# Kernel tuning notes

Hardware: AMD Instinct MI355X
Metric: run time of the kernel (lower is better)

## Reference

```python
import jax, jax.numpy as jnp
import numpy as np

B, G, S, NNZ = 64, 20000, 200000, 2000000

def setup_inputs() -> dict:
    key = jax.random.key(0)
    k1, k2, k3, k4, k5 = jax.random.split(key, 5)
    x = jax.random.normal(k1, (B, G), dtype=jnp.float32)
    # COO connectivity: row = SNP index (output), col = gene index (input)
    row = jax.random.randint(k2, (NNZ,), 0, S, dtype=jnp.int64)
    col = jax.random.randint(k3, (NNZ,), 0, G, dtype=jnp.int64)
    index = jnp.stack([row, col])  # [2, NNZ]
    W_sparse = jax.random.normal(k4, (NNZ,), dtype=jnp.float32) * 0.02
    b = jax.random.normal(k5, (S, 1), dtype=jnp.float32) * 0.02
    return {"x": x, "W_sparse": W_sparse, "b": b, "index": index, "n_SNPs": S}

def reference(x, W_sparse, b, index, n_SNPs):
    # spmm: sparse [n_SNPs, n_genes] @ x.T [n_genes, B] -> [n_SNPs, B]
    row, col = index[0], index[1]
    gathered = x.T[col] * W_sparse[:, None]            # [NNZ, B] edge contributions
    dot_prod = jax.ops.segment_sum(gathered, row, num_segments=n_SNPs)  # [S, B]
    output = dot_prod + b                              # bias broadcast over batch
    return output.T                                    # [B, n_SNPs]
```

## Files before the change

### kernel.cpp

```cpp
#include <hip/hip_runtime.h>
#include <hip/hip_bf16.h>


#define WAVE 64
#define BIN_EDGES 8192
#define CO_BITS 10
#define CO_ROWS 1024
#define NCO_MAX 256
#define CAP 11264

#define RL(v, i)  __builtin_amdgcn_readlane((int)(v), (i))
#define RLF(v, i) __int_as_float(__builtin_amdgcn_readlane(__float_as_int(v), (i)))

__device__ __forceinline__ int swz(int r, int b) {
    return (r << 6) + (b ^ (r & 63));
}

__device__ __forceinline__ unsigned short f2bf(float f) {
    unsigned u = __float_as_uint(f);
    unsigned r = (u + 0x7fffu + ((u >> 16) & 1u)) >> 16;
    return (unsigned short)r;
}

__global__ void initcur_kernel(int* __restrict__ bincur, int nc) {
    const int t = blockIdx.x * 256 + threadIdx.x;
    if (t < nc) bincur[t] = t * CAP;
}

__global__ void transpose64_kernel(const float* __restrict__ x,
                                   unsigned short* __restrict__ xTh, int G) {
    __shared__ float tile[64][65];
    const int t  = threadIdx.x;
    const int g0 = blockIdx.x * 64;
    {
        const int j  = t & 63;
        const int b0 = t >> 6;
        if (g0 + j < G) {
            #pragma unroll
            for (int it = 0; it < 16; ++it) {
                const int b = b0 + it * 4;
                tile[j][b] = x[(size_t)b * G + g0 + j];
            }
        }
    }
    __syncthreads();
    {
        const int b  = t & 63;
        const int j0 = t >> 6;
        #pragma unroll
        for (int it = 0; it < 16; ++it) {
            const int j = j0 + it * 4;
            if (g0 + j < G) xTh[(size_t)(g0 + j) * WAVE + b] = f2bf(tile[j][b]);
        }
    }
}

__global__ __launch_bounds__(256) void pass1_kernel(
        const int* __restrict__ row, const int* __restrict__ col,
        const float* __restrict__ w, int* __restrict__ bincur,
        uint2* __restrict__ sedge1, int nnz, int ncoarse) {
    __shared__ int hist[4][NCO_MAX];
    __shared__ int cb[NCO_MAX];
    __shared__ int cur[NCO_MAX];
    const int t  = threadIdx.x;
    const int wv = t >> 6;
    const int e0 = blockIdx.x * BIN_EDGES;
    const bool full = (e0 + BIN_EDGES <= nnz);
    for (int j = t; j < 4 * NCO_MAX; j += 256) ((int*)hist)[j] = 0;
    __syncthreads();
    if (full) {
        const int4* rv = (const int4*)(row + e0);
        #pragma unroll 2
        for (int k = 0; k < BIN_EDGES / 1024; ++k) {
            const int4 r4 = rv[k * 256 + t];
            atomicAdd(&hist[wv][r4.x >> CO_BITS], 1);
            atomicAdd(&hist[wv][r4.y >> CO_BITS], 1);
            atomicAdd(&hist[wv][r4.z >> CO_BITS], 1);
            atomicAdd(&hist[wv][r4.w >> CO_BITS], 1);
        }
    } else {
        for (int k = 0; k < BIN_EDGES / 256; ++k) {
            const int i = e0 + k * 256 + t;
            if (i < nnz) atomicAdd(&hist[wv][row[i] >> CO_BITS], 1);
        }
    }
    __syncthreads();
    for (int j = t; j < ncoarse; j += 256) {
        const int h = hist[0][j] + hist[1][j] + hist[2][j] + hist[3][j];
        cb[j]  = h ? atomicAdd(&bincur[j], h) : 0;
        cur[j] = 0;
    }
    __syncthreads();
    if (full) {
        const int4*   rv = (const int4*)(row + e0);
        const int4*   cv = (const int4*)(col + e0);
        const float4* wf = (const float4*)(w + e0);
        for (int k = 0; k < BIN_EDGES / 1024; ++k) {
            const int4   r4 = rv[k * 256 + t];
            const int4   c4 = cv[k * 256 + t];
            const float4 w4 = wf[k * 256 + t];
            {
                const int c = r4.x >> CO_BITS;
                const int pos = cb[c] + atomicAdd(&cur[c], 1);
                sedge1[pos] = make_uint2(((unsigned)(r4.x & (CO_ROWS - 1)) << 15) |
                                         (unsigned)c4.x, __float_as_uint(w4.x));
            }
            {
                const int c = r4.y >> CO_BITS;
                const int pos = cb[c] + atomicAdd(&cur[c], 1);
                sedge1[pos] = make_uint2(((unsigned)(r4.y & (CO_ROWS - 1)) << 15) |
                                         (unsigned)c4.y, __float_as_uint(w4.y));
            }
            {
                const int c = r4.z >> CO_BITS;
                const int pos = cb[c] + atomicAdd(&cur[c], 1);
                sedge1[pos] = make_uint2(((unsigned)(r4.z & (CO_ROWS - 1)) << 15) |
                                         (unsigned)c4.z, __float_as_uint(w4.z));
            }
            {
                const int c = r4.w >> CO_BITS;
                const int pos = cb[c] + atomicAdd(&cur[c], 1);
                sedge1[pos] = make_uint2(((unsigned)(r4.w & (CO_ROWS - 1)) << 15) |
                                         (unsigned)c4.w, __float_as_uint(w4.w));
            }
        }
    } else {
        for (int k = 0; k < BIN_EDGES / 256; ++k) {
            const int i = e0 + k * 256 + t;
            if (i < nnz) {
                const int r = row[i];
                const int c = r >> CO_BITS;
                const int pos = cb[c] + atomicAdd(&cur[c], 1);
                sedge1[pos] = make_uint2(((unsigned)(r & (CO_ROWS - 1)) << 15) |
                                         (unsigned)col[i], __float_as_uint(w[i]));
            }
        }
    }
}

__global__ __launch_bounds__(512) void pass2_kernel(
        const uint2* __restrict__ sedge1, const int* __restrict__ bincur,
        uint2* __restrict__ sedge2, int* __restrict__ rowse, int S) {
    __shared__ int rhist[CO_ROWS];
    __shared__ int sd[512];
    const int t  = threadIdx.x;
    const int c  = blockIdx.x;
    const int cs = c * CAP;
    const int M  = bincur[c] - cs;
    const int r0 = c << CO_BITS;
    const int nrows = min(CO_ROWS, S - r0);

    rhist[t] = 0;
    rhist[t + 512] = 0;
    __syncthreads();
    for (int i = t; i < M; i += 512)
        atomicAdd(&rhist[sedge1[cs + i].x >> 15], 1);
    __syncthreads();

    const int b2 = t * 2;
    const int u0 = rhist[b2], u1 = rhist[b2 + 1];
    const int s1 = u0, s2 = u0 + u1;
    sd[t] = s2;
    __syncthreads();
    for (int o = 1; o < 512; o <<= 1) {
        const int a = (t >= o) ? sd[t - o] : 0;
        __syncthreads();
        sd[t] += a;
        __syncthreads();
    }
    const int tex = sd[t] - s2;
    rhist[b2] = tex;
    rhist[b2 + 1] = tex + s1;
    if (b2 < nrows) {
        rowse[2 * (r0 + b2)]     = cs + tex;
        rowse[2 * (r0 + b2) + 1] = cs + tex + u0;
    }
    if (b2 + 1 < nrows) {
        rowse[2 * (r0 + b2 + 1)]     = cs + tex + u0;
        rowse[2 * (r0 + b2 + 1) + 1] = cs + tex + s2;
    }
    __syncthreads();

    for (int i = t; i < M; i += 512) {
        const uint2 e = sedge1[cs + i];
        const int r = (int)(e.x >> 15);
        const int pos = cs + atomicAdd(&rhist[r], 1);
        sedge2[pos] = make_uint2((e.x & 0x7fffu) << 7, e.y);
    }
}

#define PROC(Er, ar, ii)                                                      \
    {                                                                         \
        const int   k_ = RL((Er).x, (ii));                                    \
        const float w_ = __int_as_float(RL((Er).y, (ii)));                    \
        const float v_ = __uint_as_float(                                     \
            (unsigned)*(const unsigned short*)(xb + k_ + lane2) << 16);       \
        (ar) += v_ * w_;                                                      \
    }

__global__ __launch_bounds__(256) void compute_kernel(
        const unsigned short* __restrict__ xTh,
        const uint2* __restrict__ sedge,
        const int* __restrict__ rowse,
        const float* __restrict__ bias,
        float* __restrict__ out, int S) {
    __shared__ float tile[64 * 64];
    const int lane = threadIdx.x & 63;
    const int wv   = threadIdx.x >> 6;
    const int r0   = blockIdx.x * 64;
    const int rw   = r0 + wv * 16;
    const char* xb = (const char*)xTh;
    const int lane2 = lane * 2;

    int se = 0;
    if (lane < 32) se = rowse[2 * rw + lane];
    float bv = 0.f;
    if (lane < 16) bv = bias[rw + lane];

    #pragma unroll
    for (int q = 0; q < 4; ++q) {
        const int j0 = q * 4;
        int s0 = RL(se, 2*j0),     e0g = RL(se, 2*j0 + 1);
        int s1 = RL(se, 2*j0 + 2), e1g = RL(se, 2*j0 + 3);
        int s2 = RL(se, 2*j0 + 4), e2g = RL(se, 2*j0 + 5);
        int s3 = RL(se, 2*j0 + 6), e3g = RL(se, 2*j0 + 7);
        float a0 = 0.f, a1 = 0.f, a2 = 0.f, a3 = 0.f;
        while ((s0 < e0g) || (s1 < e1g) || (s2 < e2g) || (s3 < e3g)) {
            const int m0 = min(WAVE, e0g - s0);
            const int m1 = min(WAVE, e1g - s1);
            const int m2 = min(WAVE, e2g - s2);
            const int m3 = min(WAVE, e3g - s3);
            uint2 E0 = make_uint2(0u, 0u), E1 = make_uint2(0u, 0u);
            uint2 E2 = make_uint2(0u, 0u), E3 = make_uint2(0u, 0u);
            if (lane < m0) E0 = sedge[s0 + lane];
            if (lane < m1) E1 = sedge[s1 + lane];
            if (lane < m2) E2 = sedge[s2 + lane];
            if (lane < m3) E3 = sedge[s3 + lane];
            const int mm = max(max(m0, m1), max(m2, m3));
            int i = 0;
            for (; i + 2 <= mm; i += 2) {
                PROC(E0, a0, i) PROC(E1, a1, i) PROC(E2, a2, i) PROC(E3, a3, i)
                PROC(E0, a0, i + 1) PROC(E1, a1, i + 1)
                PROC(E2, a2, i + 1) PROC(E3, a3, i + 1)
            }
            if (i < mm) {
                PROC(E0, a0, i) PROC(E1, a1, i) PROC(E2, a2, i) PROC(E3, a3, i)
            }
            s0 += max(m0, 0); s1 += max(m1, 0);
            s2 += max(m2, 0); s3 += max(m3, 0);
        }
        const int rl = wv * 16 + j0;
        tile[swz(rl + 0, lane)] = a0 + RLF(bv, j0 + 0);
        tile[swz(rl + 1, lane)] = a1 + RLF(bv, j0 + 1);
        tile[swz(rl + 2, lane)] = a2 + RLF(bv, j0 + 2);
        tile[swz(rl + 3, lane)] = a3 + RLF(bv, j0 + 3);
    }
    __syncthreads();
    #pragma unroll
    for (int k = 0; k < 16; ++k) {
        const int b = wv * 16 + k;
        out[(size_t)b * S + r0 + lane] = tile[swz(lane, b)];
    }
}

extern "C" void kernel_launch(void* const* d_in, const int* in_sizes, int n_in,
                              void* d_out, int out_size, void* d_ws, size_t ws_size,
                              hipStream_t stream) {
    const float* x    = (const float*)d_in[0];
    const float* W    = (const float*)d_in[1];
    const float* bias = (const float*)d_in[2];
    const int*   idx  = (const int*)d_in[3];

    const int NNZ = in_sizes[1];
    const int S   = in_sizes[2];
    const int B   = out_size / S;
    const int G   = in_sizes[0] / B;
    const int* rowi = idx;
    const int* coli = idx + NNZ;
    float* out = (float*)d_out;

    const int ncoarse = (S + CO_ROWS - 1) >> CO_BITS;

    char* ws = (char*)d_ws;
    size_t o = 0;
    auto alloc = [&](size_t bytes) {
        void* p = ws + o;
        o = (o + bytes + 255) & ~(size_t)255;
        return p;
    };
    unsigned short* xTh = (unsigned short*)alloc((size_t)G * B * sizeof(unsigned short));
    int*   bincur = (int*)  alloc(NCO_MAX * sizeof(int));
    int*   rowse  = (int*)  alloc((size_t)2 * S * sizeof(int));
    uint2* sedge1 = (uint2*)alloc((size_t)ncoarse * CAP * sizeof(uint2));
    uint2* sedge2 = (uint2*)alloc((size_t)ncoarse * CAP * sizeof(uint2));
    (void)ws_size; (void)n_in;

    initcur_kernel<<<1, 256, 0, stream>>>(bincur, ncoarse);

    const int tgrid = (G + 63) / 64;
    transpose64_kernel<<<tgrid, 256, 0, stream>>>(x, xTh, G);

    const int bgrid = (NNZ + BIN_EDGES - 1) / BIN_EDGES;
    pass1_kernel<<<bgrid, 256, 0, stream>>>(rowi, coli, W, bincur, sedge1,
                                            NNZ, ncoarse);
    pass2_kernel<<<ncoarse, 512, 0, stream>>>(sedge1, bincur, sedge2, rowse, S);

    compute_kernel<<<S / 64, 256, 0, stream>>>(xTh, sedge2, rowse, bias,
                                               out, S);
}
```

Baseline: 185.1 us.

## Fuse row-level sort and SpMM compute into one LDS-resident kernel per coarse bin

```diff
diff --git a/kernel.cpp b/kernel.cpp
--- a/kernel.cpp
+++ b/kernel.cpp
@@ -4,13 +4,10 @@
 
 #define WAVE 64
 #define BIN_EDGES 8192
-#define CO_BITS 10
-#define CO_ROWS 1024
-#define NCO_MAX 256
-#define CAP 11264
-
-#define RL(v, i)  __builtin_amdgcn_readlane((int)(v), (i))
-#define RLF(v, i) __int_as_float(__builtin_amdgcn_readlane(__float_as_int(v), (i)))
+#define CO_BITS 8
+#define CO_ROWS 256
+#define NCO_MAX 800
+#define CAP 3072
 
 __device__ __forceinline__ int swz(int r, int b) {
     return (r << 6) + (b ^ (r & 63));
@@ -55,82 +52,84 @@
     }
 }
 
-__global__ __launch_bounds__(256) void pass1_kernel(
+__global__ __launch_bounds__(512) void pass1_kernel(
         const int* __restrict__ row, const int* __restrict__ col,
         const float* __restrict__ w, int* __restrict__ bincur,
         uint2* __restrict__ sedge1, int nnz, int ncoarse) {
-    __shared__ int hist[4][NCO_MAX];
-    __shared__ int cb[NCO_MAX];
-    __shared__ int cur[NCO_MAX];
+    __shared__ int hist[8][NCO_MAX];
     const int t  = threadIdx.x;
     const int wv = t >> 6;
     const int e0 = blockIdx.x * BIN_EDGES;
     const bool full = (e0 + BIN_EDGES <= nnz);
-    for (int j = t; j < 4 * NCO_MAX; j += 256) ((int*)hist)[j] = 0;
+    for (int j = t; j < 8 * NCO_MAX; j += 512) ((int*)hist)[j] = 0;
     __syncthreads();
     if (full) {
         const int4* rv = (const int4*)(row + e0);
-        #pragma unroll 2
-        for (int k = 0; k < BIN_EDGES / 1024; ++k) {
-            const int4 r4 = rv[k * 256 + t];
+        #pragma unroll
+        for (int k = 0; k < BIN_EDGES / 2048; ++k) {
+            const int4 r4 = rv[k * 512 + t];
             atomicAdd(&hist[wv][r4.x >> CO_BITS], 1);
             atomicAdd(&hist[wv][r4.y >> CO_BITS], 1);
             atomicAdd(&hist[wv][r4.z >> CO_BITS], 1);
             atomicAdd(&hist[wv][r4.w >> CO_BITS], 1);
         }
     } else {
-        for (int k = 0; k < BIN_EDGES / 256; ++k) {
-            const int i = e0 + k * 256 + t;
+        for (int k = 0; k < BIN_EDGES / 512; ++k) {
+            const int i = e0 + k * 512 + t;
             if (i < nnz) atomicAdd(&hist[wv][row[i] >> CO_BITS], 1);
         }
     }
     __syncthreads();
-    for (int j = t; j < ncoarse; j += 256) {
-        const int h = hist[0][j] + hist[1][j] + hist[2][j] + hist[3][j];
-        cb[j]  = h ? atomicAdd(&bincur[j], h) : 0;
-        cur[j] = 0;
+    for (int j = t; j < ncoarse; j += 512) {
+        int h[8];
+        int tot = 0;
+        #pragma unroll
+        for (int v = 0; v < 8; ++v) { h[v] = hist[v][j]; tot += h[v]; }
+        int run = tot ? atomicAdd(&bincur[j], tot) : 0;
+        #pragma unroll
+        for (int v = 0; v < 8; ++v) { hist[v][j] = run; run += h[v]; }
     }
     __syncthreads();
     if (full) {
         const int4*   rv = (const int4*)(row + e0);
         const int4*   cv = (const int4*)(col + e0);
         const float4* wf = (const float4*)(w + e0);
-        for (int k = 0; k < BIN_EDGES / 1024; ++k) {
-            const int4   r4 = rv[k * 256 + t];
-            const int4   c4 = cv[k * 256 + t];
-            const float4 w4 = wf[k * 256 + t];
+        for (int k = 0; k < BIN_EDGES / 2048; ++k) {
+            const int4   r4 = rv[k * 512 + t];
+            const int4   c4 = cv[k * 512 + t];
+            const float4 w4 = wf[k * 512 + t];
             {
                 const int c = r4.x >> CO_BITS;
-                const int pos = cb[c] + atomicAdd(&cur[c], 1);
+                const int pos = atomicAdd(&hist[wv][c], 1);
                 sedge1[pos] = make_uint2(((unsigned)(r4.x & (CO_ROWS - 1)) << 15) |
                                          (unsigned)c4.x, __float_as_uint(w4.x));
             }
             {
                 const int c = r4.y >> CO_BITS;
-                const int pos = cb[c] + atomicAdd(&cur[c], 1);
+                const int pos = atomicAdd(&hist[wv][c], 1);
                 sedge1[pos] = make_uint2(((unsigned)(r4.y & (CO_ROWS - 1)) << 15) |
                                          (unsigned)c4.y, __float_as_uint(w4.y));
             }
             {
                 const int c = r4.z >> CO_BITS;
-                const int pos = cb[c] + atomicAdd(&cur[c], 1);
+                const int pos = atomicAdd(&hist[wv][c], 1);
                 sedge1[pos] = make_uint2(((unsigned)(r4.z & (CO_ROWS - 1)) << 15) |
                                          (unsigned)c4.z, __float_as_uint(w4.z));
             }
             {
                 const int c = r4.w >> CO_BITS;
-                const int pos = cb[c] + atomicAdd(&cur[c], 1);
+                const int pos = atomicAdd(&hist[wv][c], 1);
                 sedge1[pos] = make_uint2(((unsigned)(r4.w & (CO_ROWS - 1)) << 15) |
                                          (unsigned)c4.w, __float_as_uint(w4.w));
             }
         }
     } else {
-        for (int k = 0; k < BIN_EDGES / 256; ++k) {
-            const int i = e0 + k * 256 + t;
+        for (int k = 0; k < BIN_EDGES / 512; ++k) {
+            const int i = e0 + k * 512 + t;
             if (i < nnz) {
                 const int r = row[i];
                 const int c = r >> CO_BITS;
-                const int pos = cb[c] + atomicAdd(&cur[c], 1);
+                const int pos = atomicAdd(&hist[wv][c], 1);
                 sedge1[pos] = make_uint2(((unsigned)(r & (CO_ROWS - 1)) << 15) |
                                          (unsigned)col[i], __float_as_uint(w[i]));
             }
@@ -138,128 +137,119 @@
     }
 }
 
-__global__ __launch_bounds__(512) void pass2_kernel(
-        const uint2* __restrict__ sedge1, const int* __restrict__ bincur,
-        uint2* __restrict__ sedge2, int* __restrict__ rowse, int S) {
-    __shared__ int rhist[CO_ROWS];
-    __shared__ int sd[512];
-    const int t  = threadIdx.x;
-    const int c  = blockIdx.x;
-    const int cs = c * CAP;
-    const int M  = bincur[c] - cs;
-    const int r0 = c << CO_BITS;
+#define PROCQ(nj, sj, aj, ii)                                                 \
+    {                                                                         \
+        const bool ok_ = (ii) < (nj);                                         \
+        const int idx_ = ok_ ? ((sj) + (ii)) : 0;                             \
+        const uint2 E_ = eds[idx_];                                           \
+        const unsigned k_ = ok_ ? E_.x : 0u;                                  \
+        const float w_ = ok_ ? __uint_as_float(E_.y) : 0.f;                   \
+        const float v_ = __uint_as_float(                                     \
+            (unsigned)*(const unsigned short*)(xbl + k_) << 16);              \
+        (aj) += v_ * w_;                                                      \
+    }
+
+__global__ __launch_bounds__(512) void fused_kernel(
+        const unsigned short* __restrict__ xTh,
+        const uint2* __restrict__ sedge1,
+        const int* __restrict__ bincur,
+        const float* __restrict__ bias,
+        float* __restrict__ out, int S) {
+    __shared__ uint2 eds[CAP];
+    __shared__ int   rhist[CO_ROWS];
+    __shared__ int   rstart[CO_ROWS];
+    __shared__ float bls[CO_ROWS];
+
+    const int t    = threadIdx.x;
+    const int lane = t & 63;
+    const int wv   = t >> 6;
+    const int c    = blockIdx.x;
+    const int cs   = c * CAP;
+    const int r0   = c << CO_BITS;
+    const int M    = bincur[c] - cs;
     const int nrows = min(CO_ROWS, S - r0);
 
-    rhist[t] = 0;
-    rhist[t + 512] = 0;
-    __syncthreads();
+    if (t < CO_ROWS) {
+        rhist[t] = 0;
+        bls[t] = (t < nrows) ? bias[r0 + t] : 0.f;
+    }
+    __syncthreads();
+
     for (int i = t; i < M; i += 512)
         atomicAdd(&rhist[sedge1[cs + i].x >> 15], 1);
     __syncthreads();
 
-    const int b2 = t * 2;
-    const int u0 = rhist[b2], u1 = rhist[b2 + 1];
-    const int s1 = u0, s2 = u0 + u1;
-    sd[t] = s2;
-    __syncthreads();
-    for (int o = 1; o < 512; o <<= 1) {
-        const int a = (t >= o) ? sd[t - o] : 0;
-        __syncthreads();
-        sd[t] += a;
-        __syncthreads();
-    }
-    const int tex = sd[t] - s2;
-    rhist[b2] = tex;
-    rhist[b2 + 1] = tex + s1;
-    if (b2 < nrows) {
-        rowse[2 * (r0 + b2)]     = cs + tex;
-        rowse[2 * (r0 + b2) + 1] = cs + tex + u0;
-    }
-    if (b2 + 1 < nrows) {
-        rowse[2 * (r0 + b2 + 1)]     = cs + tex + u0;
-        rowse[2 * (r0 + b2 + 1) + 1] = cs + tex + s2;
+    int cnt_t = 0;
+    if (t < CO_ROWS) { cnt_t = rhist[t]; rstart[t] = cnt_t; }
+    __syncthreads();
+    for (int o = 1; o < CO_ROWS; o <<= 1) {
+        int a = 0;
+        if (t < CO_ROWS && t >= o) a = rstart[t - o];
+        __syncthreads();
+        if (t < CO_ROWS) rstart[t] += a;
+        __syncthreads();
+    }
+    if (t < CO_ROWS) {
+        const int st = rstart[t] - cnt_t;
+        rstart[t] = st;
+        rhist[t]  = st;
     }
     __syncthreads();
 
     for (int i = t; i < M; i += 512) {
         const uint2 e = sedge1[cs + i];
         const int r = (int)(e.x >> 15);
-        const int pos = cs + atomicAdd(&rhist[r], 1);
-        sedge2[pos] = make_uint2((e.x & 0x7fffu) << 7, e.y);
-    }
-}
-
-#define PROC(Er, ar, ii)                                                      \
-    {                                                                         \
-        const int   k_ = RL((Er).x, (ii));                                    \
-        const float w_ = __int_as_float(RL((Er).y, (ii)));                    \
-        const float v_ = __uint_as_float(                                     \
-            (unsigned)*(const unsigned short*)(xb + k_ + lane2) << 16);       \
-        (ar) += v_ * w_;                                                      \
-    }
-
-__global__ __launch_bounds__(256) void compute_kernel(
-        const unsigned short* __restrict__ xTh,
-        const uint2* __restrict__ sedge,
-        const int* __restrict__ rowse,
-        const float* __restrict__ bias,
-        float* __restrict__ out, int S) {
-    __shared__ float tile[64 * 64];
-    const int lane = threadIdx.x & 63;
-    const int wv   = threadIdx.x >> 6;
-    const int r0   = blockIdx.x * 64;
-    const int rw   = r0 + wv * 16;
-    const char* xb = (const char*)xTh;
-    const int lane2 = lane * 2;
-
-    int se = 0;
-    if (lane < 32) se = rowse[2 * rw + lane];
-    float bv = 0.f;
-    if (lane < 16) bv = bias[rw + lane];
-
+        const int pos = atomicAdd(&rhist[r], 1);
+        eds[pos] = make_uint2((e.x & 0x7fffu) << 7, e.y);
+    }
+    __syncthreads();
+
+    const char* xbl = (const char*)xTh + lane * 2;
+    float acc[32];
     #pragma unroll
-    for (int q = 0; q < 4; ++q) {
-        const int j0 = q * 4;
-        int s0 = RL(se, 2*j0),     e0g = RL(se, 2*j0 + 1);
-        int s1 = RL(se, 2*j0 + 2), e1g = RL(se, 2*j0 + 3);
-        int s2 = RL(se, 2*j0 + 4), e2g = RL(se, 2*j0 + 5);
-        int s3 = RL(se, 2*j0 + 6), e3g = RL(se, 2*j0 + 7);
+    for (int q = 0; q < 8; ++q) {
+        const int rl = wv * 32 + q * 4;
+        const int s0 = rstart[rl + 0], n0 = rhist[rl + 0] - s0;
+        const int s1 = rstart[rl + 1], n1 = rhist[rl + 1] - s1;
+        const int s2 = rstart[rl + 2], n2 = rhist[rl + 2] - s2;
+        const int s3 = rstart[rl + 3], n3 = rhist[rl + 3] - s3;
         float a0 = 0.f, a1 = 0.f, a2 = 0.f, a3 = 0.f;
-        while ((s0 < e0g) || (s1 < e1g) || (s2 < e2g) || (s3 < e3g)) {
-            const int m0 = min(WAVE, e0g - s0);
-            const int m1 = min(WAVE, e1g - s1);
-            const int m2 = min(WAVE, e2g - s2);
-            const int m3 = min(WAVE, e3g - s3);
-            uint2 E0 = make_uint2(0u, 0u), E1 = make_uint2(0u, 0u);
-            uint2 E2 = make_uint2(0u, 0u), E3 = make_uint2(0u, 0u);
-            if (lane < m0) E0 = sedge[s0 + lane];
-            if (lane < m1) E1 = sedge[s1 + lane];
-            if (lane < m2) E2 = sedge[s2 + lane];
-            if (lane < m3) E3 = sedge[s3 + lane];
-            const int mm = max(max(m0, m1), max(m2, m3));
-            int i = 0;
-            for (; i + 2 <= mm; i += 2) {
-                PROC(E0, a0, i) PROC(E1, a1, i) PROC(E2, a2, i) PROC(E3, a3, i)
-                PROC(E0, a0, i + 1) PROC(E1, a1, i + 1)
-                PROC(E2, a2, i + 1) PROC(E3, a3, i + 1)
-            }
-            if (i < mm) {
-                PROC(E0, a0, i) PROC(E1, a1, i) PROC(E2, a2, i) PROC(E3, a3, i)
-            }
-            s0 += max(m0, 0); s1 += max(m1, 0);
-            s2 += max(m2, 0); s3 += max(m3, 0);
-        }
-        const int rl = wv * 16 + j0;
-        tile[swz(rl + 0, lane)] = a0 + RLF(bv, j0 + 0);
-        tile[swz(rl + 1, lane)] = a1 + RLF(bv, j0 + 1);
-        tile[swz(rl + 2, lane)] = a2 + RLF(bv, j0 + 2);
-        tile[swz(rl + 3, lane)] = a3 + RLF(bv, j0 + 3);
-    }
-    __syncthreads();
-    #pragma unroll
-    for (int k = 0; k < 16; ++k) {
-        const int b = wv * 16 + k;
-        out[(size_t)b * S + r0 + lane] = tile[swz(lane, b)];
+        const int mm = max(max(n0, n1), max(n2, n3));
+        int i = 0;
+        for (; i + 2 <= mm; i += 2) {
+            PROCQ(n0, s0, a0, i) PROCQ(n1, s1, a1, i)
+            PROCQ(n2, s2, a2, i) PROCQ(n3, s3, a3, i)
+            PROCQ(n0, s0, a0, i + 1) PROCQ(n1, s1, a1, i + 1)
+            PROCQ(n2, s2, a2, i + 1) PROCQ(n3, s3, a3, i + 1)
+        }
+        if (i < mm) {
+            PROCQ(n0, s0, a0, i) PROCQ(n1, s1, a1, i)
+            PROCQ(n2, s2, a2, i) PROCQ(n3, s3, a3, i)
+        }
+        acc[q * 4 + 0] = a0 + bls[rl + 0];
+        acc[q * 4 + 1] = a1 + bls[rl + 1];
+        acc[q * 4 + 2] = a2 + bls[rl + 2];
+        acc[q * 4 + 3] = a3 + bls[rl + 3];
+    }
+    __syncthreads();
+
+    float* tile = (float*)eds;
+    const int nblk = (nrows + 63) >> 6;
+    for (int wblk = 0; wblk < nblk; ++wblk) {
+        if ((wv >> 1) == wblk) {
+            const int half = wv & 1;
+            #pragma unroll
+            for (int k = 0; k < 32; ++k)
+                tile[swz(half * 32 + k, lane)] = acc[k];
+        }
+        __syncthreads();
+        #pragma unroll
+        for (int k = 0; k < 8; ++k) {
+            const int b = wv * 8 + k;
+            const int srow = r0 + wblk * 64 + lane;
+            if (srow < S) out[(size_t)b * S + srow] = tile[swz(lane, b)];
+        }
+        __syncthreads();
     }
 }
 
@@ -290,21 +280,18 @@
     };
     unsigned short* xTh = (unsigned short*)alloc((size_t)G * B * sizeof(unsigned short));
     int*   bincur = (int*)  alloc(NCO_MAX * sizeof(int));
-    int*   rowse  = (int*)  alloc((size_t)2 * S * sizeof(int));
     uint2* sedge1 = (uint2*)alloc((size_t)ncoarse * CAP * sizeof(uint2));
-    uint2* sedge2 = (uint2*)alloc((size_t)ncoarse * CAP * sizeof(uint2));
     (void)ws_size; (void)n_in;
 
-    initcur_kernel<<<1, 256, 0, stream>>>(bincur, ncoarse);
+    initcur_kernel<<<(ncoarse + 255) / 256, 256, 0, stream>>>(bincur, ncoarse);
 
     const int tgrid = (G + 63) / 64;
     transpose64_kernel<<<tgrid, 256, 0, stream>>>(x, xTh, G);
 
     const int bgrid = (NNZ + BIN_EDGES - 1) / BIN_EDGES;
-    pass1_kernel<<<bgrid, 256, 0, stream>>>(rowi, coli, W, bincur, sedge1,
+    pass1_kernel<<<bgrid, 512, 0, stream>>>(rowi, coli, W, bincur, sedge1,
                                             NNZ, ncoarse);
-    pass2_kernel<<<ncoarse, 512, 0, stream>>>(sedge1, bincur, sedge2, rowse, S);
-
-    compute_kernel<<<S / 64, 256, 0, stream>>>(xTh, sedge2, rowse, bias,
-                                               out, S);
-}
+
+    fused_kernel<<<ncoarse, 512, 0, stream>>>(xTh, sedge1, bincur, bias,
+                                              out, S);
+}
```

Result: slower. 219.1 us (+18.4%).

## Replace global-atomic bucket scatter with block-local LDS sort and segment table

Applied to the files above, without the earlier changes.

```diff
diff --git a/kernel.cpp b/kernel.cpp
--- a/kernel.cpp
+++ b/kernel.cpp
@@ -4,10 +4,10 @@
 
 #define WAVE 64
 #define BIN_EDGES 8192
-#define CO_BITS 10
-#define CO_ROWS 1024
-#define NCO_MAX 256
-#define CAP 11264
+#define CO_BITS 9
+#define CO_ROWS 512
+#define NCO_PAD 512
+#define CAP 5888
 
 #define RL(v, i)  __builtin_amdgcn_readlane((int)(v), (i))
 #define RLF(v, i) __int_as_float(__builtin_amdgcn_readlane(__float_as_int(v), (i)))
@@ -20,11 +20,6 @@
     unsigned u = __float_as_uint(f);
     unsigned r = (u + 0x7fffu + ((u >> 16) & 1u)) >> 16;
     return (unsigned short)r;
-}
-
-__global__ void initcur_kernel(int* __restrict__ bincur, int nc) {
-    const int t = blockIdx.x * 256 + threadIdx.x;
-    if (t < nc) bincur[t] = t * CAP;
 }
 
 __global__ void transpose64_kernel(const float* __restrict__ x,
@@ -55,137 +50,158 @@
     }
 }
 
-__global__ __launch_bounds__(256) void pass1_kernel(
+__global__ __launch_bounds__(512) void pass1_kernel(
         const int* __restrict__ row, const int* __restrict__ col,
-        const float* __restrict__ w, int* __restrict__ bincur,
-        uint2* __restrict__ sedge1, int nnz, int ncoarse) {
-    __shared__ int hist[4][NCO_MAX];
-    __shared__ int cb[NCO_MAX];
-    __shared__ int cur[NCO_MAX];
-    const int t  = threadIdx.x;
-    const int wv = t >> 6;
-    const int e0 = blockIdx.x * BIN_EDGES;
+        const float* __restrict__ w,
+        uint2* __restrict__ sedge1, uint2* __restrict__ segtab,
+        int nnz, int nco) {
+    __shared__ uint2 stage[BIN_EDGES];
+    __shared__ int hist[4][NCO_PAD];
+    __shared__ int cb[NCO_PAD];
+    const int t   = threadIdx.x;
+    const int rep = t >> 7;
+    const int e0  = blockIdx.x * BIN_EDGES;
     const bool full = (e0 + BIN_EDGES <= nnz);
-    for (int j = t; j < 4 * NCO_MAX; j += 256) ((int*)hist)[j] = 0;
-    __syncthreads();
+    const int M   = full ? BIN_EDGES : (nnz - e0);
+
+    for (int j = t; j < 4 * NCO_PAD; j += 512) ((int*)hist)[j] = 0;
+    __syncthreads();
+
     if (full) {
         const int4* rv = (const int4*)(row + e0);
-        #pragma unroll 2
-        for (int k = 0; k < BIN_EDGES / 1024; ++k) {
-            const int4 r4 = rv[k * 256 + t];
-            atomicAdd(&hist[wv][r4.x >> CO_BITS], 1);
-            atomicAdd(&hist[wv][r4.y >> CO_BITS], 1);
-            atomicAdd(&hist[wv][r4.z >> CO_BITS], 1);
-            atomicAdd(&hist[wv][r4.w >> CO_BITS], 1);
+        #pragma unroll
+        for (int k = 0; k < BIN_EDGES / 2048; ++k) {
+            const int4 r4 = rv[k * 512 + t];
+            atomicAdd(&hist[rep][r4.x >> CO_BITS], 1);
+            atomicAdd(&hist[rep][r4.y >> CO_BITS], 1);
+            atomicAdd(&hist[rep][r4.z >> CO_BITS], 1);
+            atomicAdd(&hist[rep][r4.w >> CO_BITS], 1);
         }
     } else {
-        for (int k = 0; k < BIN_EDGES / 256; ++k) {
-            const int i = e0 + k * 256 + t;
-            if (i < nnz) atomicAdd(&hist[wv][row[i] >> CO_BITS], 1);
-        }
-    }
-    __syncthreads();
-    for (int j = t; j < ncoarse; j += 256) {
-        const int h = hist[0][j] + hist[1][j] + hist[2][j] + hist[3][j];
-        cb[j]  = h ? atomicAdd(&bincur[j], h) : 0;
-        cur[j] = 0;
-    }
-    __syncthreads();
+        for (int k = 0; k < BIN_EDGES / 512; ++k) {
+            const int i = k * 512 + t;
+            if (i < M) atomicAdd(&hist[rep][row[e0 + i] >> CO_BITS], 1);
+        }
+    }
+    __syncthreads();
+
+    const int h0 = hist[0][t], h1 = hist[1][t], h2 = hist[2][t], h3 = hist[3][t];
+    const int tot = h0 + h1 + h2 + h3;
+    cb[t] = tot;
+    __syncthreads();
+    for (int o = 1; o < NCO_PAD; o <<= 1) {
+        const int a = (t >= o) ? cb[t - o] : 0;
+        __syncthreads();
+        cb[t] += a;
+        __syncthreads();
+    }
+    const int excl = cb[t] - tot;
+    if (t < nco)
+        segtab[(size_t)blockIdx.x * nco + t] =
+            make_uint2((unsigned)(e0 + excl), (unsigned)tot);
+    {
+        int run = excl;
+        hist[0][t] = run; run += h0;
+        hist[1][t] = run; run += h1;
+        hist[2][t] = run; run += h2;
+        hist[3][t] = run;
+    }
+    __syncthreads();
+
     if (full) {
         const int4*   rv = (const int4*)(row + e0);
         const int4*   cv = (const int4*)(col + e0);
         const float4* wf = (const float4*)(w + e0);
-        for (int k = 0; k < BIN_EDGES / 1024; ++k) {
-            const int4   r4 = rv[k * 256 + t];
-            const int4   c4 = cv[k * 256 + t];
-            const float4 w4 = wf[k * 256 + t];
+        #pragma unroll
+        for (int k = 0; k < BIN_EDGES / 2048; ++k) {
+            const int4   r4 = rv[k * 512 + t];
+            const int4   c4 = cv[k * 512 + t];
+            const float4 w4 = wf[k * 512 + t];
             {
-                const int c = r4.x >> CO_BITS;
-                const int pos = cb[c] + atomicAdd(&cur[c], 1);
-                sedge1[pos] = make_uint2(((unsigned)(r4.x & (CO_ROWS - 1)) << 15) |
-                                         (unsigned)c4.x, __float_as_uint(w4.x));
+                const int pos = atomicAdd(&hist[rep][r4.x >> CO_BITS], 1);
+                stage[pos] = make_uint2(((unsigned)(r4.x & (CO_ROWS - 1)) << 15) |
+                                        (unsigned)c4.x, __float_as_uint(w4.x));
             }
             {
-                const int c = r4.y >> CO_BITS;
-                const int pos = cb[c] + atomicAdd(&cur[c], 1);
-                sedge1[pos] = make_uint2(((unsigned)(r4.y & (CO_ROWS - 1)) << 15) |
-                                         (unsigned)c4.y, __float_as_uint(w4.y));
+                const int pos = atomicAdd(&hist[rep][r4.y >> CO_BITS], 1);
+                stage[pos] = make_uint2(((unsigned)(r4.y & (CO_ROWS - 1)) << 15) |
+                                        (unsigned)c4.y, __float_as_uint(w4.y));
             }
             {
-                const int c = r4.z >> CO_BITS;
-                const int pos = cb[c] + atomicAdd(&cur[c], 1);
-                sedge1[pos] = make_uint2(((unsigned)(r4.z & (CO_ROWS - 1)) << 15) |
-                                         (unsigned)c4.z, __float_as_uint(w4.z));
+                const int pos = atomicAdd(&hist[rep][r4.z >> CO_BITS], 1);
+                stage[pos] = make_uint2(((unsigned)(r4.z & (CO_ROWS - 1)) << 15) |
+                                        (unsigned)c4.z, __float_as_uint(w4.z));
             }
             {
-                const int c = r4.w >> CO_BITS;
-                const int pos = cb[c] + atomicAdd(&cur[c], 1);
-                sedge1[pos] = make_uint2(((unsigned)(r4.w & (CO_ROWS - 1)) << 15) |
-                                         (unsigned)c4.w, __float_as_uint(w4.w));
+                const int pos = atomicAdd(&hist[rep][r4.w >> CO_BITS], 1);
+                stage[pos] = make_uint2(((unsigned)(r4.w & (CO_ROWS - 1)) << 15) |
+                                        (unsigned)c4.w, __float_as_uint(w4.w));
             }
         }
     } else {
-        for (int k = 0; k < BIN_EDGES / 256; ++k) {
-            const int i = e0 + k * 256 + t;
-            if (i < nnz) {
-                const int r = row[i];
-                const int c = r >> CO_BITS;
-                const int pos = cb[c] + atomicAdd(&cur[c], 1);
-                sedge1[pos] = make_uint2(((unsigned)(r & (CO_ROWS - 1)) << 15) |
-                                         (unsigned)col[i], __float_as_uint(w[i]));
-            }
-        }
-    }
+        for (int k = 0; k < BIN_EDGES / 512; ++k) {
+            const int i = k * 512 + t;
+            if (i < M) {
+                const int r = row[e0 + i];
+                const int pos = atomicAdd(&hist[rep][r >> CO_BITS], 1);
+                stage[pos] = make_uint2(((unsigned)(r & (CO_ROWS - 1)) << 15) |
+                                        (unsigned)col[e0 + i],
+                                        __float_as_uint(w[e0 + i]));
+            }
+        }
+    }
+    __syncthreads();
+
+    for (int j = t; j < M; j += 512) sedge1[e0 + j] = stage[j];
 }
 
 __global__ __launch_bounds__(512) void pass2_kernel(
-        const uint2* __restrict__ sedge1, const int* __restrict__ bincur,
-        uint2* __restrict__ sedge2, int* __restrict__ rowse, int S) {
+        const uint2* __restrict__ sedge1, const uint2* __restrict__ segtab,
+        uint2* __restrict__ sedge2, int* __restrict__ rowse,
+        int S, int nblk, int nco) {
     __shared__ int rhist[CO_ROWS];
-    __shared__ int sd[512];
+    __shared__ int rs[CO_ROWS];
     const int t  = threadIdx.x;
     const int c  = blockIdx.x;
     const int cs = c * CAP;
-    const int M  = bincur[c] - cs;
     const int r0 = c << CO_BITS;
     const int nrows = min(CO_ROWS, S - r0);
 
     rhist[t] = 0;
-    rhist[t + 512] = 0;
-    __syncthreads();
-    for (int i = t; i < M; i += 512)
-        atomicAdd(&rhist[sedge1[cs + i].x >> 15], 1);
-    __syncthreads();
-
-    const int b2 = t * 2;
-    const int u0 = rhist[b2], u1 = rhist[b2 + 1];
-    const int s1 = u0, s2 = u0 + u1;
-    sd[t] = s2;
-    __syncthreads();
-    for (int o = 1; o < 512; o <<= 1) {
-        const int a = (t >= o) ? sd[t - o] : 0;
+    __syncthreads();
+
+    for (int s = t >> 1; s < nblk; s += 256) {
+        const uint2 sg = segtab[(size_t)s * nco + c];
+        for (int i = t & 1; i < (int)sg.y; i += 2)
+            atomicAdd(&rhist[(int)(sedge1[sg.x + i].x >> 15)], 1);
+    }
+    __syncthreads();
+
+    const int cnt = rhist[t];
+    rs[t] = cnt;
+    __syncthreads();
+    for (int o = 1; o < CO_ROWS; o <<= 1) {
+        const int a = (t >= o) ? rs[t - o] : 0;
         __syncthreads();
-        sd[t] += a;
+        rs[t] += a;
         __syncthreads();
     }
-    const int tex = sd[t] - s2;
-    rhist[b2] = tex;
-    rhist[b2 + 1] = tex + s1;
-    if (b2 < nrows) {
-        rowse[2 * (r0 + b2)]     = cs + tex;
-        rowse[2 * (r0 + b2) + 1] = cs + tex + u0;
-    }
-    if (b2 + 1 < nrows) {
-        rowse[2 * (r0 + b2 + 1)]     = cs + tex + u0;
-        rowse[2 * (r0 + b2 + 1) + 1] = cs + tex + s2;
-    }
-    __syncthreads();
-
-    for (int i = t; i < M; i += 512) {
-        const uint2 e = sedge1[cs + i];
-        const int r = (int)(e.x >> 15);
-        const int pos = cs + atomicAdd(&rhist[r], 1);
-        sedge2[pos] = make_uint2((e.x & 0x7fffu) << 7, e.y);
+    const int excl = rs[t] - cnt;
+    if (t < nrows) {
+        rowse[2 * (r0 + t)]     = cs + excl;
+        rowse[2 * (r0 + t) + 1] = cs + excl + cnt;
+    }
+    rhist[t] = excl;
+    __syncthreads();
+
+    for (int s = t >> 1; s < nblk; s += 256) {
+        const uint2 sg = segtab[(size_t)s * nco + c];
+        for (int i = t & 1; i < (int)sg.y; i += 2) {
+            const uint2 e = sedge1[sg.x + i];
+            const int r = (int)(e.x >> 15);
+            const int pos = atomicAdd(&rhist[r], 1);
+            sedge2[cs + pos] = make_uint2((e.x & 0x7fffu) << 7, e.y);
+        }
     }
 }
 
@@ -279,7 +295,8 @@
     const int* coli = idx + NNZ;
     float* out = (float*)d_out;
 
-    const int ncoarse = (S + CO_ROWS - 1) >> CO_BITS;
+    const int nco  = (S + CO_ROWS - 1) >> CO_BITS;
+    const int nblk = (NNZ + BIN_EDGES - 1) / BIN_EDGES;
 
     char* ws = (char*)d_ws;
     size_t o = 0;
@@ -289,22 +306,19 @@
         return p;
     };
     unsigned short* xTh = (unsigned short*)alloc((size_t)G * B * sizeof(unsigned short));
-    int*   bincur = (int*)  alloc(NCO_MAX * sizeof(int));
+    uint2* sedge1 = (uint2*)alloc((size_t)NNZ * sizeof(uint2));
+    uint2* sedge2 = (uint2*)alloc((size_t)nco * CAP * sizeof(uint2));
+    uint2* segtab = (uint2*)alloc((size_t)nblk * nco * sizeof(uint2));
     int*   rowse  = (int*)  alloc((size_t)2 * S * sizeof(int));
-    uint2* sedge1 = (uint2*)alloc((size_t)ncoarse * CAP * sizeof(uint2));
-    uint2* sedge2 = (uint2*)alloc((size_t)ncoarse * CAP * sizeof(uint2));
     (void)ws_size; (void)n_in;
-
-    initcur_kernel<<<1, 256, 0, stream>>>(bincur, ncoarse);
 
     const int tgrid = (G + 63) / 64;
     transpose64_kernel<<<tgrid, 256, 0, stream>>>(x, xTh, G);
 
-    const int bgrid = (NNZ + BIN_EDGES - 1) / BIN_EDGES;
-    pass1_kernel<<<bgrid, 256, 0, stream>>>(rowi, coli, W, bincur, sedge1,
-                                            NNZ, ncoarse);
-    pass2_kernel<<<ncoarse, 512, 0, stream>>>(sedge1, bincur, sedge2, rowse, S);
-
+    pass1_kernel<<<nblk, 512, 0, stream>>>(rowi, coli, W, sedge1, segtab,
+                                           NNZ, nco);
+    pass2_kernel<<<nco, 512, 0, stream>>>(sedge1, segtab, sedge2, rowse,
+                                          S, nblk, nco);
     compute_kernel<<<S / 64, 256, 0, stream>>>(xTh, sedge2, rowse, bias,
                                                out, S);
 }
```

New measurement: 180.1 us. 1.03x faster.
